# Optimization experiments

Measured on AMD Instinct MI355X. Metric: run time of the kernel, lower is better.

The kernel has to match this reference:

```python
import jax, jax.numpy as jnp
import numpy as np

B, LQ, LK, D_WORD, D_K, D_V = 8, 2048, 2048, 1024, 128, 128
TEMPERATURE = 11.313708498984761  # sqrt(d_k)
NEG_BIG = -1e9


def setup_inputs() -> dict:
    key = jax.random.key(0)
    ks = jax.random.split(key, 7)
    scale = 1.0 / np.sqrt(D_WORD)
    return {
        "q": jax.random.normal(ks[0], (B, LQ, D_WORD), dtype=jnp.float32),
        "k": jax.random.normal(ks[1], (B, LK, D_WORD), dtype=jnp.float32),
        "v": jax.random.normal(ks[2], (B, LK, D_WORD), dtype=jnp.float32),
        "memory_lengths": jax.random.randint(ks[3], (B,), 1, LK + 1, dtype=jnp.int32),
        "Wq": jax.random.normal(ks[4], (D_WORD, D_K), dtype=jnp.float32) * scale,
        "Wk": jax.random.normal(ks[5], (D_WORD, D_K), dtype=jnp.float32) * scale,
        "Wv": jax.random.normal(ks[6], (D_WORD, D_V), dtype=jnp.float32) * scale,
    }


def reference(q, k, v, memory_lengths, Wq, Wk, Wv):
    # Projections (bias-free Dense layers)
    qs = jnp.einsum("bqw,wd->bqd", q, Wq)   # [B, LQ, D_K]
    ks = jnp.einsum("bkw,wd->bkd", k, Wk)   # [B, LK, D_K]
    vs = jnp.einsum("bkw,wd->bkd", v, Wv)   # [B, LK, D_V]
    # Scaled dot-product scores
    attn = jnp.einsum("bqd,bkd->bqk", qs, ks) / TEMPERATURE  # [B, LQ, LK]
    # Padding mask from memory_lengths (tf.sequence_mask + tile + where)
    mem_mask = jnp.arange(attn.shape[-1])[None, None, :] < memory_lengths[:, None, None]
    attn = jnp.where(mem_mask, attn, NEG_BIG)
    p = jax.nn.softmax(attn, axis=-1)
    return jnp.einsum("bqk,bkd->bqd", p, vs)  # [B, LQ, D_V]
```

## Files before the change

### kernel.cpp

```cpp
#include <hip/hip_runtime.h>

typedef _Float16 half8 __attribute__((ext_vector_type(8)));
typedef float floatx4 __attribute__((ext_vector_type(4)));

#define INV_TEMP 0.08838834764831845f

#define OFF_WT 0
#define OFF_QS (786432)
#define OFF_KS (786432 + 4194304)
#define OFF_VT (786432 + 2 * 4194304)

__global__ __launch_bounds__(256) void wprep_kernel(
    const float* __restrict__ Wq, const float* __restrict__ Wk,
    const float* __restrict__ Wv, _Float16* __restrict__ wt)
{
    __shared__ _Float16 T[64 * 136];
    const int t = threadIdx.x;
    const int kt = blockIdx.x;
    const int m = blockIdx.y;
    const float* W = (m == 0) ? Wq : (m == 1) ? Wk : Wv;
    const float scale = (m == 0) ? INV_TEMP : 1.0f;
    const float* src = W + kt * 8192;

    #pragma unroll
    for (int i = 0; i < 8; i++) {
        int f = i * 1024 + t * 4;
        float4 v = *(const float4*)(src + f);
        int k = f >> 7, n = f & 127;
        _Float16* d = T + k * 136 + n;
        d[0] = (_Float16)(v.x * scale);
        d[1] = (_Float16)(v.y * scale);
        d[2] = (_Float16)(v.z * scale);
        d[3] = (_Float16)(v.w * scale);
    }
    __syncthreads();

    _Float16* dst = wt + m * 131072 + kt * 8192;
    #pragma unroll
    for (int i = 0; i < 4; i++) {
        int p = i * 256 + t;
        int n = p >> 3;
        int c = (p & 7) ^ (n & 7);
        half8 h;
        #pragma unroll
        for (int j = 0; j < 8; j++)
            h[j] = T[(c * 8 + j) * 136 + n];
        *(half8*)(dst + p * 8) = h;
    }
}

__global__ __launch_bounds__(256) void proj_kernel(
    const float* __restrict__ Xq, const float* __restrict__ Xk,
    const float* __restrict__ Xv, const _Float16* __restrict__ wt,
    _Float16* __restrict__ qs, _Float16* __restrict__ ks,
    _Float16* __restrict__ vt)
{
    __shared__ _Float16 Bs[2][8192];

    const int t = threadIdx.x;
    const int lane = t & 63;
    const int w = t >> 6;
    const int quad = lane >> 4;
    const int m16 = lane & 15;
    const int yb = blockIdx.y;
    const float* X = (yb == 0) ? Xq : (yb == 1) ? Xk : Xv;
    const _Float16* W = wt + yb * 131072;
    const int m0 = blockIdx.x * 64;
    const int row = m0 + w * 16 + m16;
    const float* arow = X + (size_t)row * 1024;

    floatx4 acc[8] = {};

    const int sw0 = (quad) ^ (m16 & 7);
    const int sw1 = (4 + quad) ^ (m16 & 7);

    auto stageB = [&](int buf, int kt) {
        const _Float16* src = W + kt * 8192;
        #pragma unroll
        for (int i = 0; i < 4; i++) {
            int slotbase = (w * 4 + i) * 64;
            __builtin_amdgcn_global_load_lds(
                (const __attribute__((address_space(1))) unsigned int*)(src + (size_t)(slotbase + lane) * 8),
                (__attribute__((address_space(3))) unsigned int*)(&Bs[buf][(slotbase + lane) * 8]),
                16, 0, 0);
        }
    };

    stageB(0, 0);
    float4 a0 = *(const float4*)(arow + quad * 8);
    float4 a1 = *(const float4*)(arow + quad * 8 + 4);
    float4 a2 = *(const float4*)(arow + 32 + quad * 8);
    float4 a3 = *(const float4*)(arow + 32 + quad * 8 + 4);
    __builtin_amdgcn_s_waitcnt(0);
    __syncthreads();

    for (int kt = 0; kt < 16; kt++) {
        const int cur = kt & 1;
        float4 n0, n1, n2, n3;
        if (kt < 15) {
            stageB(cur ^ 1, kt + 1);
            const float* na = arow + (kt + 1) * 64;
            n0 = *(const float4*)(na + quad * 8);
            n1 = *(const float4*)(na + quad * 8 + 4);
            n2 = *(const float4*)(na + 32 + quad * 8);
            n3 = *(const float4*)(na + 32 + quad * 8 + 4);
        }

        half8 af0 = {(_Float16)a0.x, (_Float16)a0.y, (_Float16)a0.z, (_Float16)a0.w,
                     (_Float16)a1.x, (_Float16)a1.y, (_Float16)a1.z, (_Float16)a1.w};
        half8 af1 = {(_Float16)a2.x, (_Float16)a2.y, (_Float16)a2.z, (_Float16)a2.w,
                     (_Float16)a3.x, (_Float16)a3.y, (_Float16)a3.z, (_Float16)a3.w};

        const char* bb = (const char*)&Bs[cur][0];
        #pragma unroll
        for (int nt = 0; nt < 8; nt++) {
            half8 bf = *(const half8*)(bb + (nt * 16 + m16) * 128 + sw0 * 16);
            acc[nt] = __builtin_amdgcn_mfma_f32_16x16x32_f16(af0, bf, acc[nt], 0, 0, 0);
        }
        #pragma unroll
        for (int nt = 0; nt < 8; nt++) {
            half8 bf = *(const half8*)(bb + (nt * 16 + m16) * 128 + sw1 * 16);
            acc[nt] = __builtin_amdgcn_mfma_f32_16x16x32_f16(af1, bf, acc[nt], 0, 0, 0);
        }

        a0 = n0; a1 = n1; a2 = n2; a3 = n3;
        __builtin_amdgcn_s_waitcnt(0);
        __syncthreads();
    }

    if (yb < 2) {
        _Float16* out = (yb == 0) ? qs : ks;
        #pragma unroll
        for (int nt = 0; nt < 8; nt++) {
            #pragma unroll
            for (int r = 0; r < 4; r++) {
                int orow = m0 + w * 16 + quad * 4 + r;
                out[(size_t)orow * 128 + nt * 16 + m16] = (_Float16)acc[nt][r];
            }
        }
    } else {
        _Float16* T = &Bs[0][0];
        #pragma unroll
        for (int nt = 0; nt < 8; nt++) {
            #pragma unroll
            for (int r = 0; r < 4; r++)
                T[(w * 16 + quad * 4 + r) * 130 + nt * 16 + m16] = (_Float16)acc[nt][r];
        }
        __syncthreads();
        int dv = t >> 1, hf = t & 1;
        int bb2 = m0 >> 11;
        int key0 = (m0 & 2047) + hf * 32;
        _Float16* dst = vt + (size_t)(bb2 * 128 + dv) * 2048 + key0;
        #pragma unroll
        for (int j8 = 0; j8 < 4; j8++) {
            half8 h;
            #pragma unroll
            for (int j = 0; j < 8; j++)
                h[j] = T[(hf * 32 + j8 * 8 + j) * 130 + dv];
            *(half8*)(dst + j8 * 8) = h;
        }
    }
}

__global__ __launch_bounds__(256) void attn_kernel(
    const _Float16* __restrict__ qs, const _Float16* __restrict__ ks,
    const _Float16* __restrict__ vt, const int* __restrict__ mlen,
    float* __restrict__ out)
{
    __shared__ _Float16 kls[64 * 136];
    __shared__ _Float16 vls[128 * 72];
    __shared__ _Float16 pls[4 * 16 * 72];

    const int t = threadIdx.x;
    const int lane = t & 63;
    const int w = t >> 6;
    const int quad = lane >> 4;
    const int m16 = lane & 15;
    const int b = blockIdx.y;
    const int q0 = blockIdx.x * 64;
    const int ml = mlen[b];
    const int nkt = (ml + 63) >> 6;

    half8 aq[4];
    {
        const _Float16* qrow =
            qs + (size_t)(b * 2048 + q0 + w * 16 + m16) * 128 + quad * 8;
        #pragma unroll
        for (int d = 0; d < 4; d++)
            aq[d] = *(const half8*)(qrow + d * 32);
    }

    floatx4 acc[8] = {};
    float m_i[4] = {-3e38f, -3e38f, -3e38f, -3e38f};
    float l_i[4] = {0.f, 0.f, 0.f, 0.f};

    const int skey = t >> 2, sq4 = t & 3;
    const int sdv = t >> 1, shf = t & 1;

    for (int kt = 0; kt < nkt; kt++) {
        const int k0 = kt * 64;
        {
            const _Float16* src = ks + (size_t)(b * 2048 + k0 + skey) * 128 + sq4 * 32;
            _Float16* dst = kls + skey * 136 + sq4 * 32;
            #pragma unroll
            for (int i = 0; i < 4; i++)
                *(half8*)(dst + 8 * i) = ((const half8*)src)[i];
        }
        {
            const _Float16* src = vt + (size_t)(b * 128 + sdv) * 2048 + k0 + shf * 32;
            _Float16* dst = vls + sdv * 72 + shf * 32;
            #pragma unroll
            for (int i = 0; i < 4; i++)
                *(half8*)(dst + 8 * i) = ((const half8*)src)[i];
        }
        __syncthreads();

        floatx4 sacc[4] = {};
        #pragma unroll
        for (int d = 0; d < 4; d++) {
            #pragma unroll
            for (int nt = 0; nt < 4; nt++) {
                half8 bfrag = *(const half8*)(kls + (nt * 16 + m16) * 136 + d * 32 + quad * 8);
                sacc[nt] = __builtin_amdgcn_mfma_f32_16x16x32_f16(aq[d], bfrag, sacc[nt], 0, 0, 0);
            }
        }

        float p[4][4];
        float rowmax[4], rowsum[4];
        #pragma unroll
        for (int r = 0; r < 4; r++) rowmax[r] = -3e38f;
        #pragma unroll
        for (int nt = 0; nt < 4; nt++) {
            int key = k0 + nt * 16 + m16;
            bool valid = key < ml;
            #pragma unroll
            for (int r = 0; r < 4; r++) {
                float s = valid ? sacc[nt][r] : -3e38f;
                p[nt][r] = s;
                rowmax[r] = fmaxf(rowmax[r], s);
            }
        }
        #pragma unroll
        for (int mask = 8; mask >= 1; mask >>= 1) {
            #pragma unroll
            for (int r = 0; r < 4; r++)
                rowmax[r] = fmaxf(rowmax[r], __shfl_xor(rowmax[r], mask, 64));
        }
        #pragma unroll
        for (int r = 0; r < 4; r++) {
            float mnew = fmaxf(m_i[r], rowmax[r]);
            float alpha = __expf(m_i[r] - mnew);
            m_i[r] = mnew;
            l_i[r] *= alpha;
            #pragma unroll
            for (int nt = 0; nt < 8; nt++) acc[nt][r] *= alpha;
            rowsum[r] = 0.f;
            #pragma unroll
            for (int nt = 0; nt < 4; nt++) {
                float e = __expf(p[nt][r] - mnew);
                p[nt][r] = e;
                rowsum[r] += e;
            }
        }
        #pragma unroll
        for (int mask = 8; mask >= 1; mask >>= 1) {
            #pragma unroll
            for (int r = 0; r < 4; r++)
                rowsum[r] += __shfl_xor(rowsum[r], mask, 64);
        }
        #pragma unroll
        for (int r = 0; r < 4; r++) l_i[r] += rowsum[r];

        _Float16* pw = pls + w * 16 * 72;
        #pragma unroll
        for (int nt = 0; nt < 4; nt++) {
            #pragma unroll
            for (int r = 0; r < 4; r++)
                pw[(quad * 4 + r) * 72 + nt * 16 + m16] = (_Float16)p[nt][r];
        }
        __syncthreads();

        #pragma unroll
        for (int kp = 0; kp < 2; kp++) {
            half8 pa = *(const half8*)(pw + m16 * 72 + kp * 32 + quad * 8);
            #pragma unroll
            for (int nt = 0; nt < 8; nt++) {
                half8 bfrag = *(const half8*)(vls + (nt * 16 + m16) * 72 + kp * 32 + quad * 8);
                acc[nt] = __builtin_amdgcn_mfma_f32_16x16x32_f16(pa, bfrag, acc[nt], 0, 0, 0);
            }
        }
        __syncthreads();
    }

    #pragma unroll
    for (int r = 0; r < 4; r++) {
        float inv_l = 1.0f / l_i[r];
        int orow = b * 2048 + q0 + w * 16 + quad * 4 + r;
        float* dst = out + (size_t)orow * 128;
        #pragma unroll
        for (int nt = 0; nt < 8; nt++)
            dst[nt * 16 + m16] = acc[nt][r] * inv_l;
    }
}

extern "C" void kernel_launch(void* const* d_in, const int* in_sizes, int n_in,
                              void* d_out, int out_size, void* d_ws, size_t ws_size,
                              hipStream_t stream) {
    const float* q   = (const float*)d_in[0];
    const float* k   = (const float*)d_in[1];
    const float* v   = (const float*)d_in[2];
    const int* mlen  = (const int*)d_in[3];
    const float* Wq  = (const float*)d_in[4];
    const float* Wk  = (const float*)d_in[5];
    const float* Wv  = (const float*)d_in[6];
    float* out = (float*)d_out;

    char* ws = (char*)d_ws;
    _Float16* wt = (_Float16*)(ws + OFF_WT);
    _Float16* qs = (_Float16*)(ws + OFF_QS);
    _Float16* kss = (_Float16*)(ws + OFF_KS);
    _Float16* vt = (_Float16*)(ws + OFF_VT);

    hipLaunchKernelGGL(wprep_kernel, dim3(16, 3), dim3(256), 0, stream, Wq, Wk, Wv, wt);
    hipLaunchKernelGGL(proj_kernel, dim3(256, 3), dim3(256), 0, stream,
                       q, k, v, wt, qs, kss, vt);
    hipLaunchKernelGGL(attn_kernel, dim3(32, 8), dim3(256), 0, stream,
                       qs, kss, vt, mlen, out);
}
```

Measured before the change: 289.0 us.

## Split-K attention with pre-tiled swizzled K/V, async LDS loads, and merge pass

Projection now stages X tiles into LDS via async global_load_lds with bigger k-steps. K and V are written as pre-swizzled 64-key tiles so the attention kernel can load them into double-buffered LDS asynchronously. The attention kernel optionally splits the key range in two along a grid z-dimension, writing partial accumulators plus max/sum, and a merge kernel combines them. This raises parallelism, since only 256 blocks ran before, and overlaps loads with compute. The cost is an extra partial-buffer round trip through memory and one more launch.

```diff
diff --git a/kernel.cpp b/kernel.cpp
--- a/kernel.cpp
+++ b/kernel.cpp
@@ -5,10 +5,12 @@
 
 #define INV_TEMP 0.08838834764831845f
 
-#define OFF_WT 0
-#define OFF_QS (786432)
-#define OFF_KS (786432 + 4194304)
-#define OFF_VT (786432 + 2 * 4194304)
+#define OFF_WT   0
+#define OFF_QS   786432
+#define OFF_KT   (786432 + 4194304)
+#define OFF_VT   (OFF_KT + 4194304)
+#define OFF_PART (OFF_VT + 4194304)
+#define PART_BYTES (2ull * 8 * 2048 * 132 * 4)
 
 __global__ __launch_bounds__(256) void wprep_kernel(
     const float* __restrict__ Wq, const float* __restrict__ Wk,
@@ -52,10 +54,11 @@
 __global__ __launch_bounds__(256) void proj_kernel(
     const float* __restrict__ Xq, const float* __restrict__ Xk,
     const float* __restrict__ Xv, const _Float16* __restrict__ wt,
-    _Float16* __restrict__ qs, _Float16* __restrict__ ks,
-    _Float16* __restrict__ vt)
+    _Float16* __restrict__ qs, _Float16* __restrict__ ks_t,
+    _Float16* __restrict__ vt_t)
 {
-    __shared__ _Float16 Bs[2][8192];
+    __shared__ float As[64 * 128];
+    __shared__ _Float16 Bs[2 * 8192];
 
     const int t = threadIdx.x;
     const int lane = t & 63;
@@ -66,80 +69,88 @@
     const float* X = (yb == 0) ? Xq : (yb == 1) ? Xk : Xv;
     const _Float16* W = wt + yb * 131072;
     const int m0 = blockIdx.x * 64;
-    const int row = m0 + w * 16 + m16;
-    const float* arow = X + (size_t)row * 1024;
 
     floatx4 acc[8] = {};
-
-    const int sw0 = (quad) ^ (m16 & 7);
-    const int sw1 = (4 + quad) ^ (m16 & 7);
-
-    auto stageB = [&](int buf, int kt) {
-        const _Float16* src = W + kt * 8192;
-        #pragma unroll
-        for (int i = 0; i < 4; i++) {
-            int slotbase = (w * 4 + i) * 64;
-            __builtin_amdgcn_global_load_lds(
-                (const __attribute__((address_space(1))) unsigned int*)(src + (size_t)(slotbase + lane) * 8),
-                (__attribute__((address_space(3))) unsigned int*)(&Bs[buf][(slotbase + lane) * 8]),
-                16, 0, 0);
-        }
-    };
-
-    stageB(0, 0);
-    float4 a0 = *(const float4*)(arow + quad * 8);
-    float4 a1 = *(const float4*)(arow + quad * 8 + 4);
-    float4 a2 = *(const float4*)(arow + 32 + quad * 8);
-    float4 a3 = *(const float4*)(arow + 32 + quad * 8 + 4);
-    __builtin_amdgcn_s_waitcnt(0);
-    __syncthreads();
-
-    for (int kt = 0; kt < 16; kt++) {
-        const int cur = kt & 1;
-        float4 n0, n1, n2, n3;
-        if (kt < 15) {
-            stageB(cur ^ 1, kt + 1);
-            const float* na = arow + (kt + 1) * 64;
-            n0 = *(const float4*)(na + quad * 8);
-            n1 = *(const float4*)(na + quad * 8 + 4);
-            n2 = *(const float4*)(na + 32 + quad * 8);
-            n3 = *(const float4*)(na + 32 + quad * 8 + 4);
-        }
-
-        half8 af0 = {(_Float16)a0.x, (_Float16)a0.y, (_Float16)a0.z, (_Float16)a0.w,
-                     (_Float16)a1.x, (_Float16)a1.y, (_Float16)a1.z, (_Float16)a1.w};
-        half8 af1 = {(_Float16)a2.x, (_Float16)a2.y, (_Float16)a2.z, (_Float16)a2.w,
-                     (_Float16)a3.x, (_Float16)a3.y, (_Float16)a3.z, (_Float16)a3.w};
-
-        const char* bb = (const char*)&Bs[cur][0];
-        #pragma unroll
-        for (int nt = 0; nt < 8; nt++) {
-            half8 bf = *(const half8*)(bb + (nt * 16 + m16) * 128 + sw0 * 16);
-            acc[nt] = __builtin_amdgcn_mfma_f32_16x16x32_f16(af0, bf, acc[nt], 0, 0, 0);
-        }
-        #pragma unroll
-        for (int nt = 0; nt < 8; nt++) {
-            half8 bf = *(const half8*)(bb + (nt * 16 + m16) * 128 + sw1 * 16);
-            acc[nt] = __builtin_amdgcn_mfma_f32_16x16x32_f16(af1, bf, acc[nt], 0, 0, 0);
-        }
-
-        a0 = n0; a1 = n1; a2 = n2; a3 = n3;
+    const int e = m16 & 7;
+
+    for (int s = 0; s < 8; s++) {
+        if (s) __syncthreads();
+        {
+            const float* base = X + (size_t)m0 * 1024 + s * 128;
+            #pragma unroll
+            for (int i = 0; i < 8; i++) {
+                int st = i * 256 + t;
+                int row = st >> 5;
+                int p = st & 31;
+                int c = (p & 24) | ((p & 7) ^ (row & 7));
+                __builtin_amdgcn_global_load_lds(
+                    (const __attribute__((address_space(1))) unsigned int*)(base + (size_t)row * 1024 + c * 4),
+                    (__attribute__((address_space(3))) unsigned int*)(As + st * 4),
+                    16, 0, 0);
+            }
+        }
+        {
+            const _Float16* src = W + s * 16384;
+            #pragma unroll
+            for (int i = 0; i < 8; i++) {
+                int slot = (w * 8 + i) * 64 + lane;
+                __builtin_amdgcn_global_load_lds(
+                    (const __attribute__((address_space(1))) unsigned int*)(src + (size_t)slot * 8),
+                    (__attribute__((address_space(3))) unsigned int*)(Bs + slot * 8),
+                    16, 0, 0);
+            }
+        }
         __builtin_amdgcn_s_waitcnt(0);
         __syncthreads();
-    }
-
-    if (yb < 2) {
-        _Float16* out = (yb == 0) ? qs : ks;
+
+        const float* ap = As + (w * 16 + m16) * 128;
+        #pragma unroll
+        for (int ks = 0; ks < 2; ks++) {
+            const char* bt = (const char*)(Bs + ks * 8192);
+            #pragma unroll
+            for (int hf2 = 0; hf2 < 2; hf2++) {
+                int b16 = ks * 16 + hf2 * 8;
+                float4 fa = *(const float4*)(ap + (b16 + ((quad * 2) ^ e)) * 4);
+                float4 fb = *(const float4*)(ap + (b16 + ((quad * 2 + 1) ^ e)) * 4);
+                half8 af = {(_Float16)fa.x, (_Float16)fa.y, (_Float16)fa.z, (_Float16)fa.w,
+                            (_Float16)fb.x, (_Float16)fb.y, (_Float16)fb.z, (_Float16)fb.w};
+                int sw = (hf2 * 4 + quad) ^ e;
+                #pragma unroll
+                for (int nt = 0; nt < 8; nt++) {
+                    half8 bf = *(const half8*)(bt + (nt * 16 + m16) * 128 + sw * 16);
+                    acc[nt] = __builtin_amdgcn_mfma_f32_16x16x32_f16(af, bf, acc[nt], 0, 0, 0);
+                }
+            }
+        }
+    }
+
+    const int b = m0 >> 11;
+    const int kt = (m0 & 2047) >> 6;
+
+    if (yb == 0) {
         #pragma unroll
         for (int nt = 0; nt < 8; nt++) {
             #pragma unroll
             for (int r = 0; r < 4; r++) {
                 int orow = m0 + w * 16 + quad * 4 + r;
-                out[(size_t)orow * 128 + nt * 16 + m16] = (_Float16)acc[nt][r];
+                qs[(size_t)orow * 128 + nt * 16 + m16] = (_Float16)acc[nt][r];
+            }
+        }
+    } else if (yb == 1) {
+        _Float16* tile = ks_t + (size_t)(b * 32 + kt) * 8192;
+        #pragma unroll
+        for (int nt = 0; nt < 8; nt++) {
+            #pragma unroll
+            for (int r = 0; r < 4; r++) {
+                int row = w * 16 + quad * 4 + r;
+                int col = nt * 16 + m16;
+                int p = row * 16 + ((col >> 3) ^ (row & 7));
+                tile[p * 8 + (col & 7)] = (_Float16)acc[nt][r];
             }
         }
     } else {
-        _Float16* T = &Bs[0][0];
+        __syncthreads();
+        _Float16* T = (_Float16*)As;
         #pragma unroll
         for (int nt = 0; nt < 8; nt++) {
             #pragma unroll
@@ -148,27 +159,27 @@
         }
         __syncthreads();
         int dv = t >> 1, hf = t & 1;
-        int bb2 = m0 >> 11;
-        int key0 = (m0 & 2047) + hf * 32;
-        _Float16* dst = vt + (size_t)(bb2 * 128 + dv) * 2048 + key0;
+        _Float16* tile = vt_t + (size_t)(b * 32 + kt) * 8192;
         #pragma unroll
         for (int j8 = 0; j8 < 4; j8++) {
+            int k8 = hf * 4 + j8;
             half8 h;
             #pragma unroll
             for (int j = 0; j < 8; j++)
-                h[j] = T[(hf * 32 + j8 * 8 + j) * 130 + dv];
-            *(half8*)(dst + j8 * 8) = h;
+                h[j] = T[(k8 * 8 + j) * 130 + dv];
+            int p = dv * 8 + (k8 ^ (dv & 7));
+            *(half8*)(tile + p * 8) = h;
         }
     }
 }
 
 __global__ __launch_bounds__(256) void attn_kernel(
-    const _Float16* __restrict__ qs, const _Float16* __restrict__ ks,
-    const _Float16* __restrict__ vt, const int* __restrict__ mlen,
-    float* __restrict__ out)
+    const _Float16* __restrict__ qs, const _Float16* __restrict__ ks_t,
+    const _Float16* __restrict__ vt_t, const int* __restrict__ mlen,
+    float* __restrict__ out, float* __restrict__ part, int ns)
 {
-    __shared__ _Float16 kls[64 * 136];
-    __shared__ _Float16 vls[128 * 72];
+    __shared__ _Float16 kbuf[2 * 8192];
+    __shared__ _Float16 vbuf[2 * 8192];
     __shared__ _Float16 pls[4 * 16 * 72];
 
     const int t = threadIdx.x;
@@ -177,9 +188,13 @@
     const int quad = lane >> 4;
     const int m16 = lane & 15;
     const int b = blockIdx.y;
+    const int h = blockIdx.z;
     const int q0 = blockIdx.x * 64;
     const int ml = mlen[b];
     const int nkt = (ml + 63) >> 6;
+    const int hs = (nkt + ns - 1) / ns;
+    const int kb0 = h * hs;
+    const int kb1 = min(nkt, (h + 1) * hs);
 
     half8 aq[4];
     {
@@ -194,113 +209,154 @@
     float m_i[4] = {-3e38f, -3e38f, -3e38f, -3e38f};
     float l_i[4] = {0.f, 0.f, 0.f, 0.f};
 
-    const int skey = t >> 2, sq4 = t & 3;
-    const int sdv = t >> 1, shf = t & 1;
-
-    for (int kt = 0; kt < nkt; kt++) {
-        const int k0 = kt * 64;
-        {
-            const _Float16* src = ks + (size_t)(b * 2048 + k0 + skey) * 128 + sq4 * 32;
-            _Float16* dst = kls + skey * 136 + sq4 * 32;
-            #pragma unroll
-            for (int i = 0; i < 4; i++)
-                *(half8*)(dst + 8 * i) = ((const half8*)src)[i];
-        }
-        {
-            const _Float16* src = vt + (size_t)(b * 128 + sdv) * 2048 + k0 + shf * 32;
-            _Float16* dst = vls + sdv * 72 + shf * 32;
-            #pragma unroll
-            for (int i = 0; i < 4; i++)
-                *(half8*)(dst + 8 * i) = ((const half8*)src)[i];
-        }
+    auto stage = [&](int buf, int kt) {
+        const _Float16* ksrc = ks_t + (size_t)(b * 32 + kt) * 8192;
+        const _Float16* vsrc = vt_t + (size_t)(b * 32 + kt) * 8192;
+        #pragma unroll
+        for (int i = 0; i < 4; i++) {
+            int slot = (w * 4 + i) * 64 + lane;
+            __builtin_amdgcn_global_load_lds(
+                (const __attribute__((address_space(1))) unsigned int*)(ksrc + (size_t)slot * 8),
+                (__attribute__((address_space(3))) unsigned int*)(kbuf + buf * 8192 + slot * 8),
+                16, 0, 0);
+            __builtin_amdgcn_global_load_lds(
+                (const __attribute__((address_space(1))) unsigned int*)(vsrc + (size_t)slot * 8),
+                (__attribute__((address_space(3))) unsigned int*)(vbuf + buf * 8192 + slot * 8),
+                16, 0, 0);
+        }
+    };
+
+    if (kb0 < kb1) {
+        stage(0, kb0);
+        __builtin_amdgcn_s_waitcnt(0);
         __syncthreads();
 
-        floatx4 sacc[4] = {};
-        #pragma unroll
-        for (int d = 0; d < 4; d++) {
+        for (int kt = kb0; kt < kb1; kt++) {
+            const int cur = (kt - kb0) & 1;
+            if (kt + 1 < kb1) stage(cur ^ 1, kt + 1);
+
+            const _Float16* kb = kbuf + cur * 8192;
+            const _Float16* vb = vbuf + cur * 8192;
+            const int k0 = kt * 64;
+
+            floatx4 sacc[4] = {};
+            #pragma unroll
+            for (int d = 0; d < 4; d++) {
+                #pragma unroll
+                for (int nt = 0; nt < 4; nt++) {
+                    int row = nt * 16 + m16;
+                    int p = row * 16 + ((d * 4 + quad) ^ (row & 7));
+                    half8 bf = *(const half8*)(kb + p * 8);
+                    sacc[nt] = __builtin_amdgcn_mfma_f32_16x16x32_f16(aq[d], bf, sacc[nt], 0, 0, 0);
+                }
+            }
+
+            float p4[4][4];
+            float rowmax[4], rowsum[4];
+            #pragma unroll
+            for (int r = 0; r < 4; r++) rowmax[r] = -3e38f;
             #pragma unroll
             for (int nt = 0; nt < 4; nt++) {
-                half8 bfrag = *(const half8*)(kls + (nt * 16 + m16) * 136 + d * 32 + quad * 8);
-                sacc[nt] = __builtin_amdgcn_mfma_f32_16x16x32_f16(aq[d], bfrag, sacc[nt], 0, 0, 0);
-            }
-        }
-
-        float p[4][4];
-        float rowmax[4], rowsum[4];
-        #pragma unroll
-        for (int r = 0; r < 4; r++) rowmax[r] = -3e38f;
-        #pragma unroll
-        for (int nt = 0; nt < 4; nt++) {
-            int key = k0 + nt * 16 + m16;
-            bool valid = key < ml;
+                int key = k0 + nt * 16 + m16;
+                bool valid = key < ml;
+                #pragma unroll
+                for (int r = 0; r < 4; r++) {
+                    float s = valid ? sacc[nt][r] : -3e38f;
+                    p4[nt][r] = s;
+                    rowmax[r] = fmaxf(rowmax[r], s);
+                }
+            }
+            #pragma unroll
+            for (int mask = 8; mask >= 1; mask >>= 1) {
+                #pragma unroll
+                for (int r = 0; r < 4; r++)
+                    rowmax[r] = fmaxf(rowmax[r], __shfl_xor(rowmax[r], mask, 64));
+            }
             #pragma unroll
             for (int r = 0; r < 4; r++) {
-                float s = valid ? sacc[nt][r] : -3e38f;
-                p[nt][r] = s;
-                rowmax[r] = fmaxf(rowmax[r], s);
-            }
-        }
-        #pragma unroll
-        for (int mask = 8; mask >= 1; mask >>= 1) {
-            #pragma unroll
-            for (int r = 0; r < 4; r++)
-                rowmax[r] = fmaxf(rowmax[r], __shfl_xor(rowmax[r], mask, 64));
-        }
+                float mnew = fmaxf(m_i[r], rowmax[r]);
+                float alpha = __expf(m_i[r] - mnew);
+                m_i[r] = mnew;
+                l_i[r] *= alpha;
+                #pragma unroll
+                for (int nt = 0; nt < 8; nt++) acc[nt][r] *= alpha;
+                rowsum[r] = 0.f;
+                #pragma unroll
+                for (int nt = 0; nt < 4; nt++) {
+                    float ee = __expf(p4[nt][r] - mnew);
+                    p4[nt][r] = ee;
+                    rowsum[r] += ee;
+                }
+            }
+            #pragma unroll
+            for (int mask = 8; mask >= 1; mask >>= 1) {
+                #pragma unroll
+                for (int r = 0; r < 4; r++)
+                    rowsum[r] += __shfl_xor(rowsum[r], mask, 64);
+            }
+            #pragma unroll
+            for (int r = 0; r < 4; r++) l_i[r] += rowsum[r];
+
+            _Float16* pw = pls + w * 16 * 72;
+            #pragma unroll
+            for (int nt = 0; nt < 4; nt++) {
+                #pragma unroll
+                for (int r = 0; r < 4; r++)
+                    pw[(quad * 4 + r) * 72 + nt * 16 + m16] = (_Float16)p4[nt][r];
+            }
+
+            #pragma unroll
+            for (int kp = 0; kp < 2; kp++) {
+                half8 pa = *(const half8*)(pw + m16 * 72 + kp * 32 + quad * 8);
+                #pragma unroll
+                for (int nt = 0; nt < 8; nt++) {
+                    int dv = nt * 16 + m16;
+                    int p = dv * 8 + ((kp * 4 + quad) ^ (dv & 7));
+                    half8 bf = *(const half8*)(vb + p * 8);
+                    acc[nt] = __builtin_amdgcn_mfma_f32_16x16x32_f16(pa, bf, acc[nt], 0, 0, 0);
+                }
+            }
+
+            __builtin_amdgcn_s_waitcnt(0);
+            __syncthreads();
+        }
+    }
+
+    if (ns == 1) {
         #pragma unroll
         for (int r = 0; r < 4; r++) {
-            float mnew = fmaxf(m_i[r], rowmax[r]);
-            float alpha = __expf(m_i[r] - mnew);
-            m_i[r] = mnew;
-            l_i[r] *= alpha;
-            #pragma unroll
-            for (int nt = 0; nt < 8; nt++) acc[nt][r] *= alpha;
-            rowsum[r] = 0.f;
-            #pragma unroll
-            for (int nt = 0; nt < 4; nt++) {
-                float e = __expf(p[nt][r] - mnew);
-                p[nt][r] = e;
-                rowsum[r] += e;
-            }
-        }
-        #pragma unroll
-        for (int mask = 8; mask >= 1; mask >>= 1) {
-            #pragma unroll
-            for (int r = 0; r < 4; r++)
-                rowsum[r] += __shfl_xor(rowsum[r], mask, 64);
-        }
-        #pragma unroll
-        for (int r = 0; r < 4; r++) l_i[r] += rowsum[r];
-
-        _Float16* pw = pls + w * 16 * 72;
-        #pragma unroll
-        for (int nt = 0; nt < 4; nt++) {
-            #pragma unroll
-            for (int r = 0; r < 4; r++)
-                pw[(quad * 4 + r) * 72 + nt * 16 + m16] = (_Float16)p[nt][r];
-        }
-        __syncthreads();
-
-        #pragma unroll
-        for (int kp = 0; kp < 2; kp++) {
-            half8 pa = *(const half8*)(pw + m16 * 72 + kp * 32 + quad * 8);
-            #pragma unroll
-            for (int nt = 0; nt < 8; nt++) {
-                half8 bfrag = *(const half8*)(vls + (nt * 16 + m16) * 72 + kp * 32 + quad * 8);
-                acc[nt] = __builtin_amdgcn_mfma_f32_16x16x32_f16(pa, bfrag, acc[nt], 0, 0, 0);
-            }
-        }
-        __syncthreads();
-    }
-
-    #pragma unroll
-    for (int r = 0; r < 4; r++) {
-        float inv_l = 1.0f / l_i[r];
-        int orow = b * 2048 + q0 + w * 16 + quad * 4 + r;
-        float* dst = out + (size_t)orow * 128;
-        #pragma unroll
-        for (int nt = 0; nt < 8; nt++)
-            dst[nt * 16 + m16] = acc[nt][r] * inv_l;
-    }
+            float inv_l = 1.0f / l_i[r];
+            int orow = b * 2048 + q0 + w * 16 + quad * 4 + r;
+            float* dst = out + (size_t)orow * 128;
+            #pragma unroll
+            for (int nt = 0; nt < 8; nt++)
+                dst[nt * 16 + m16] = acc[nt][r] * inv_l;
+        }
+    } else {
+        #pragma unroll
+        for (int r = 0; r < 4; r++) {
+            float* pr = part +
+                (size_t)(h * 16384 + b * 2048 + q0 + w * 16 + quad * 4 + r) * 132;
+            #pragma unroll
+            for (int nt = 0; nt < 8; nt++)
+                pr[nt * 16 + m16] = acc[nt][r];
+            if (m16 == 0) { pr[128] = m_i[r]; pr[129] = l_i[r]; }
+        }
+    }
+}
+
+__global__ __launch_bounds__(256) void merge_kernel(
+    const float* __restrict__ part, float* __restrict__ out)
+{
+    int idx = blockIdx.x * 256 + threadIdx.x;
+    int row = idx >> 7, c = idx & 127;
+    const float* p1 = part + (size_t)row * 132;
+    const float* p2 = part + (size_t)(16384 + row) * 132;
+    float m1 = p1[128], l1 = p1[129];
+    float m2 = p2[128], l2 = p2[129];
+    float M = fmaxf(m1, m2);
+    float s1 = __expf(m1 - M), s2 = __expf(m2 - M);
+    out[idx] = (p1[c] * s1 + p2[c] * s2) / (l1 * s1 + l2 * s2);
 }
 
 extern "C" void kernel_launch(void* const* d_in, const int* in_sizes, int n_in,
@@ -316,14 +372,19 @@
     float* out = (float*)d_out;
 
     char* ws = (char*)d_ws;
-    _Float16* wt = (_Float16*)(ws + OFF_WT);
-    _Float16* qs = (_Float16*)(ws + OFF_QS);
-    _Float16* kss = (_Float16*)(ws + OFF_KS);
-    _Float16* vt = (_Float16*)(ws + OFF_VT);
+    _Float16* wt   = (_Float16*)(ws + OFF_WT);
+    _Float16* qs   = (_Float16*)(ws + OFF_QS);
+    _Float16* ks_t = (_Float16*)(ws + OFF_KT);
+    _Float16* vt_t = (_Float16*)(ws + OFF_VT);
+    float* part    = (float*)(ws + OFF_PART);
+
+    const int ns = (ws_size >= (size_t)OFF_PART + PART_BYTES) ? 2 : 1;
 
     hipLaunchKernelGGL(wprep_kernel, dim3(16, 3), dim3(256), 0, stream, Wq, Wk, Wv, wt);
     hipLaunchKernelGGL(proj_kernel, dim3(256, 3), dim3(256), 0, stream,
-                       q, k, v, wt, qs, kss, vt);
-    hipLaunchKernelGGL(attn_kernel, dim3(32, 8), dim3(256), 0, stream,
-                       qs, kss, vt, mlen, out);
-}
+                       q, k, v, wt, qs, ks_t, vt_t);
+    hipLaunchKernelGGL(attn_kernel, dim3(32, 8, ns), dim3(256), 0, stream,
+                       qs, ks_t, vt_t, mlen, out, part, ns);
+    if (ns == 2)
+        hipLaunchKernelGGL(merge_kernel, dim3(8192), dim3(256), 0, stream, part, out);
+}
```

Result: faster. 259.7 us (-10.2%).
